# Kernel optimization log

Measured on AMD Instinct MI355X. Metric: run time of the kernel, lower is better.

The kernel has to match this reference:

```python
import jax, jax.numpy as jnp
import numpy as np

D, R, C = 4, 6, 32
P = 2 * R + 1          # 13 (both pixel patch and memory patch, since memory_patch_R == R)
N = P * P              # 169
DIL_INT = 15


def corr_sampler(f1, f2, p, dil):
    """SpatialCorrelationSampler(kernel_size=1, patch_size=p, dilation_patch=dil).
    out[b,i,j,y,x] = sum_c f1[b,c,y,x] * f2[b,c, y+(i-Rp)*dil, x+(j-Rp)*dil] (zero pad)."""
    Rp = (p - 1) // 2
    pad = Rp * dil
    b, c, h, w = f1.shape
    f2p = jnp.pad(f2, ((0, 0), (0, 0), (pad, pad), (pad, pad)))
    outs = [jnp.einsum('bchw,bchw->bhw', f1, f2p[:, :, i * dil:i * dil + h, j * dil:j * dil + w])
            for i in range(p) for j in range(p)]
    return jnp.stack(outs, 1).reshape(b, p, p, h, w)


def bilinear_gather(im, ys, xs):
    """Bilinear sample im [b,c,H,W] at float coords ys,xs [b,N,h,w]; zeros outside."""
    H, W = im.shape[2], im.shape[3]
    y0 = jnp.floor(ys)
    x0 = jnp.floor(xs)
    wy = ys - y0
    wx = xs - x0

    def g(yi, xi):
        valid = ((yi >= 0) & (yi < H) & (xi >= 0) & (xi < W)).astype(im.dtype)
        yc = jnp.clip(yi, 0, H - 1).astype(jnp.int32)
        xc = jnp.clip(xi, 0, W - 1).astype(jnp.int32)
        out = jax.vmap(lambda imb, yb, xb: imb[:, yb, xb])(im, yc, xc)  # [b,c,N,h,w]
        return out * valid[:, None]

    return (g(y0, x0) * ((1 - wy) * (1 - wx))[:, None]
            + g(y0, x0 + 1) * ((1 - wy) * wx)[:, None]
            + g(y0 + 1, x0) * (wy * (1 - wx))[:, None]
            + g(y0 + 1, x0 + 1) * (wy * wx)[:, None])


def deform_im2col(im, offset, p):
    """Deformable im2col: for each output pixel (y,x) and kernel pos (ky,kx),
    bilinearly sample im at (y+ky-Rp+off_y, x+kx-Rp+off_x). offset [...,0]=x, [...,1]=y.
    Returns [b,c,p*p,h,w]."""
    b, c, h, w = im.shape
    Rp = (p - 1) // 2
    ky, kx = jnp.meshgrid(jnp.arange(p) - Rp, jnp.arange(p) - Rp, indexing='ij')
    ky = ky.reshape(-1).astype(im.dtype)
    kx = kx.reshape(-1).astype(im.dtype)
    ys = (jnp.arange(h, dtype=im.dtype)[None, None, :, None]
          + ky[None, :, None, None] + offset[..., 1][:, None])  # [b,N,h,w]
    xs = (jnp.arange(w, dtype=im.dtype)[None, None, None, :]
          + kx[None, :, None, None] + offset[..., 0][:, None])
    return bilinear_gather(im, ys, xs)


def unfold_patches(x, p, pad):
    """F.unfold(kernel_size=p, padding=pad) -> [b,c,p*p,h,w]."""
    b, c, h, w = x.shape
    xp = jnp.pad(x, ((0, 0), (0, 0), (pad, pad), (pad, pad)))
    cols = [xp[:, :, i:i + h, j:j + w] for i in range(p) for j in range(p)]
    return jnp.stack(cols, 2)


def _forward(feats_r, feats_t, quantized_r, ref_index, current_ind):
    ri = np.asarray(ref_index)
    ci = int(current_ind)
    diffs = [ci - int(x) for x in ri]
    nsearch = sum(1 for d in diffs if d > DIL_INT)
    dirates = [min(4, d // DIL_INT + 1) for d in diffs if d > DIL_INT]
    nref = feats_r.shape[0]
    b, c, h, w = feats_t.shape

    # offset grid: _y,_x = meshgrid(ij) so grid[...,0]=x-offset, grid[...,1]=y-offset
    _y, _x = jnp.meshgrid(jnp.arange(-R, R + 1), jnp.arange(-R, R + 1), indexing='ij')
    grid = jnp.stack([_x, _y], -1).astype(feats_t.dtype)  # [P,P,2]

    corrs_pixel = []
    offset0 = []
    for s in range(nsearch):
        cc = corr_sampler(feats_t, feats_r[s], P, dirates[s])             # [b,P,P,h,w]
        soft = jax.nn.softmax(cc.reshape(b, N, h * w), axis=1).reshape(b, P, P, h, w)
        off = jnp.einsum('bijhw,ijd->bhwd', soft, grid) * dirates[s]      # [b,h,w,2]
        offset0.append(off)
        col0 = deform_im2col(feats_r[s], off, P)                          # [b,c,N,h,w]
        corrs_pixel.append(jnp.einsum('bchw,bcnhw->bnhw', feats_t, col0).reshape(b, N, h * w))
    for ind in range(nsearch, nref):
        corrs_pixel.append(corr_sampler(feats_t, feats_r[ind], P, 1).reshape(b, N, h * w))

    corr_pixel = jax.nn.softmax(jnp.concatenate(corrs_pixel, 1), axis=1)  # [b,nref*N,h*w]

    # prep: float + stride-D subsampling (C-channel input, so no one-hot branch)
    qr = [quantized_r[i][:, :, ::D, ::D] for i in range(nref)]            # [b,C,h,w]
    cols = [deform_im2col(qr[i], offset0[i], P).reshape(b, C, N, h * w) for i in range(nsearch)]
    cols += [unfold_patches(qr[i], P, R).reshape(b, C, N, h * w) for i in range(nsearch, nref)]
    image_uf = jnp.concatenate(cols, 2)                                   # [b,C,nref*N,h*w]

    out = jnp.einsum('bkl,bckl->bcl', corr_pixel, image_uf).reshape(b, C, h, w)
    return out


def setup_inputs() -> dict:
    key = jax.random.key(0)
    k1, k2, k3 = jax.random.split(key, 3)
    feats_r = jax.random.normal(k1, (3, 1, 64, 56, 56), jnp.float32) * 0.2
    feats_t = jax.random.normal(k2, (1, 64, 56, 56), jnp.float32) * 0.2
    quantized_r = jax.random.uniform(k3, (3, 1, 32, 224, 224), jnp.float32)
    return {
        'feats_r': feats_r,
        'feats_t': feats_t,
        'quantized_r': quantized_r,
        'ref_index': np.array([0, 30, 39], dtype=np.int64),
        'current_ind': 40,
    }


def reference(feats_r, feats_t, quantized_r, ref_index, current_ind):
    return _forward(feats_r, feats_t, quantized_r, ref_index, current_ind)
```

## Files before the change

### kernel.cpp

```cpp
#include <hip/hip_runtime.h>

#define HW   56
#define NPIX 3136
#define CH   64
#define CQ   32
#define PS   13
#define NPOS 169
#define GS   14
#define NG   196

typedef __attribute__((ext_vector_type(8))) short short8;
typedef __attribute__((ext_vector_type(4))) float f32x4;

__device__ inline float warpMax(float v) {
#pragma unroll
  for (int o = 32; o > 0; o >>= 1) v = fmaxf(v, __shfl_xor(v, o));
  return v;
}
__device__ inline float warpSum(float v) {
#pragma unroll
  for (int o = 32; o > 0; o >>= 1) v += __shfl_xor(v, o);
  return v;
}
__device__ inline ushort f2bf(float f) {
  unsigned u = __float_as_uint(f);
  return (ushort)((u + 0x7fffu + ((u >> 16) & 1u)) >> 16);
}

__global__ __launch_bounds__(256) void prep_all(
    const float* __restrict__ ft_in,
    const float* __restrict__ fr_in,
    const float* __restrict__ q_in,
    ushort* __restrict__ ft_out,
    ushort* __restrict__ fr_out,
    float* __restrict__ qout,
    float* __restrict__ zrow) {
  __shared__ float smem[CQ * (HW + 1)];
  int bid = blockIdx.x, tid = threadIdx.x;
  if (bid < 784) {
    if (bid == 0 && tid < 64) zrow[tid] = 0.f;
    int m = bid / 196, t = bid - m * 196;
    int row0 = (t / 98) * 32;
    int col0 = (t - (t / 98) * 98) * 32;
    const float* src = (m == 0) ? ft_in : fr_in + (size_t)(m - 1) * CH * NPIX;
    ushort* dst      = (m == 0) ? ft_out : fr_out + (size_t)(m - 1) * NPIX * CH;
    int tx = tid & 31, ty = tid >> 5;
    for (int r = ty; r < 32; r += 8)
      smem[r * 33 + tx] = src[(size_t)(row0 + r) * NPIX + col0 + tx];
    __syncthreads();
    for (int r = ty; r < 32; r += 8)
      dst[(size_t)(col0 + r) * CH + row0 + tx] = f2bf(smem[tx * 33 + r]);
  } else {
    int q = bid - 784;
    int r = q / HW, yy = q - r * HW;
    for (int idx = tid; idx < CQ * HW; idx += 256) {
      int c = idx / HW, xx = idx - c * HW;
      smem[c * (HW + 1) + xx] = q_in[((size_t)(r * CQ + c) * 224 + yy * 4) * 224 + xx * 4];
    }
    __syncthreads();
    for (int idx = tid; idx < CQ * HW; idx += 256) {
      int xx = idx >> 5, c = idx & 31;
      qout[(size_t)r * NPIX * CQ + (size_t)(yy * HW + xx) * CQ + c] = smem[c * (HW + 1) + xx];
    }
  }
}

__global__ __launch_bounds__(256, 6) void colorizer_main(
    const ushort* __restrict__ ftb,
    const ushort* __restrict__ frb,
    const float*  __restrict__ qr,
    const ushort* __restrict__ zrow,
    float* __restrict__ out)
{
  __shared__ float s_cc[176];
  __shared__ float s_e[528];
  __shared__ float s_D[208];
  __shared__ float s_wg[224];
  __shared__ int   s_offg[224];
  __shared__ int   s_off2[192];
  __shared__ f32x4 s_pf[32];
  __shared__ float r_max1[4], r_sum1[12], r_max2[4], r_sum2[4];

  int pix = blockIdx.x;
  int y = pix / HW, x = pix - y * HW;
  int tid = threadIdx.x;
  int wid = tid >> 6, lane = tid & 63;
  int mrow = lane & 15;
  int klane = lane >> 4;

  if (tid < 16) { s_offg[208 + tid] = -1; s_off2[176 + tid] = -1; }

  const ushort* frb0 = frb;
  const ushort* frb1 = frb + (size_t)NPIX * CH;
  const ushort* frb2 = frb + (size_t)2 * NPIX * CH;
  const f32x4* qr0v = (const f32x4*)qr;
  const f32x4* qr1v = qr0v + (size_t)NPIX * 8;
  const f32x4* qr2v = qr0v + (size_t)2 * NPIX * 8;

  const ushort* fb = ftb + (size_t)pix * CH;
  const ushort* plo = (mrow == 0) ? (fb + klane * 8) : zrow;
  const ushort* phi = (mrow == 0) ? (fb + 32 + klane * 8) : zrow;
  short8 b_lo = *(const short8*)plo;
  short8 b_hi = *(const short8*)phi;

  for (int g = wid; g < 11; g += 4) {
    int d = g * 16 + mrow;
    int ii = d / PS, jj = d - ii * PS;
    int sy1 = y + (ii - 6) * 3, sx1 = x + (jj - 6) * 3;
    int sy2 = y + ii - 6,        sx2 = x + jj - 6;
    bool dv = d < NPOS;
    bool v1 = dv && ((unsigned)sy1 < HW) && ((unsigned)sx1 < HW);
    bool v2 = dv && ((unsigned)sy2 < HW) && ((unsigned)sx2 < HW);
    int ro2 = sy2 * HW + sx2;
    const ushort* rb0 = v1 ? (frb0 + (size_t)(sy1 * HW + sx1) * CH) : zrow;
    const ushort* rb1 = v2 ? (frb1 + (size_t)ro2 * CH) : zrow;
    const ushort* rb2 = v2 ? (frb2 + (size_t)ro2 * CH) : zrow;
    short8 a0lo = *(const short8*)(rb0 + klane * 8);
    short8 a0hi = *(const short8*)(rb0 + 32 + klane * 8);
    short8 a1lo = *(const short8*)(rb1 + klane * 8);
    short8 a1hi = *(const short8*)(rb1 + 32 + klane * 8);
    short8 a2lo = *(const short8*)(rb2 + klane * 8);
    short8 a2hi = *(const short8*)(rb2 + 32 + klane * 8);
    f32x4 acc0 = {0.f, 0.f, 0.f, 0.f}, acc1 = acc0, acc2 = acc0;
    acc0 = __builtin_amdgcn_mfma_f32_16x16x32_bf16(a0lo, b_lo, acc0, 0, 0, 0);
    acc0 = __builtin_amdgcn_mfma_f32_16x16x32_bf16(a0hi, b_hi, acc0, 0, 0, 0);
    acc1 = __builtin_amdgcn_mfma_f32_16x16x32_bf16(a1lo, b_lo, acc1, 0, 0, 0);
    acc1 = __builtin_amdgcn_mfma_f32_16x16x32_bf16(a1hi, b_hi, acc1, 0, 0, 0);
    acc2 = __builtin_amdgcn_mfma_f32_16x16x32_bf16(a2lo, b_lo, acc2, 0, 0, 0);
    acc2 = __builtin_amdgcn_mfma_f32_16x16x32_bf16(a2hi, b_hi, acc2, 0, 0, 0);
    if (klane == 0) s_off2[d] = v2 ? ro2 : -1;
    if (mrow == 0) {
      *(f32x4*)&s_cc[g * 16 + klane * 4]        = acc0;
      *(f32x4*)&s_e[176 + g * 16 + klane * 4]   = acc1;
      *(f32x4*)&s_e[352 + g * 16 + klane * 4]   = acc2;
    }
  }
  __syncthreads();

  int pi = tid / PS, pj = tid - (tid / PS) * PS;
  float cc = (tid < NPOS) ? s_cc[tid] : -1e30f;
  float wmx = warpMax(cc);
  if (lane == 0) r_max1[wid] = wmx;
  __syncthreads();
  float m1 = fmaxf(fmaxf(r_max1[0], r_max1[1]), fmaxf(r_max1[2], r_max1[3]));
  float e1 = (tid < NPOS) ? __expf(cc - m1) : 0.f;
  float a0 = warpSum(e1);
  float a1 = warpSum((tid < NPOS) ? e1 * (float)(pj - 6) : 0.f);
  float a2 = warpSum((tid < NPOS) ? e1 * (float)(pi - 6) : 0.f);
  if (lane == 0) { r_sum1[wid] = a0; r_sum1[4 + wid] = a1; r_sum1[8 + wid] = a2; }
  __syncthreads();
  float se  = r_sum1[0] + r_sum1[1] + r_sum1[2] + r_sum1[3];
  float sxe = r_sum1[4] + r_sum1[5] + r_sum1[6] + r_sum1[7];
  float sye = r_sum1[8] + r_sum1[9] + r_sum1[10] + r_sum1[11];
  float offx = 3.f * sxe / se;
  float offy = 3.f * sye / se;

  float fy0 = floorf(offy), fx0 = floorf(offx);
  int   iy0 = (int)fy0,     ix0 = (int)fx0;
  float wy = offy - fy0,    wx = offx - fx0;
  float w00 = (1.f - wy) * (1.f - wx), w01 = (1.f - wy) * wx;
  float w10 = wy * (1.f - wx),         w11 = wy * wx;

  for (int g = wid; g < 13; g += 8) {
    int gB = g + 4;
    bool hasB = gB < 13;
    int d = g * 16 + mrow;
    int a = d / GS, bq = d - a * GS;
    int sy = y + iy0 + a - 6, sx = x + ix0 + bq - 6;
    bool vA = (d < NG) && ((unsigned)sy < HW) && ((unsigned)sx < HW);
    int roA = sy * HW + sx;
    const ushort* rbA = vA ? (frb0 + (size_t)roA * CH) : zrow;
    int dB = gB * 16 + mrow;
    int aB = dB / GS, bB = dB - aB * GS;
    int syB = y + iy0 + aB - 6, sxB = x + ix0 + bB - 6;
    bool vB = hasB && (dB < NG) && ((unsigned)syB < HW) && ((unsigned)sxB < HW);
    int roB = syB * HW + sxB;
    const ushort* rbB = vB ? (frb0 + (size_t)roB * CH) : zrow;
    short8 aAlo = *(const short8*)(rbA + klane * 8);
    short8 aAhi = *(const short8*)(rbA + 32 + klane * 8);
    short8 aBlo = *(const short8*)(rbB + klane * 8);
    short8 aBhi = *(const short8*)(rbB + 32 + klane * 8);
    f32x4 accA = {0.f, 0.f, 0.f, 0.f}, accB = accA;
    accA = __builtin_amdgcn_mfma_f32_16x16x32_bf16(aAlo, b_lo, accA, 0, 0, 0);
    accA = __builtin_amdgcn_mfma_f32_16x16x32_bf16(aAhi, b_hi, accA, 0, 0, 0);
    accB = __builtin_amdgcn_mfma_f32_16x16x32_bf16(aBlo, b_lo, accB, 0, 0, 0);
    accB = __builtin_amdgcn_mfma_f32_16x16x32_bf16(aBhi, b_hi, accB, 0, 0, 0);
    if (klane == 0) s_offg[d] = vA ? roA : -1;
    if (mrow == 0) *(f32x4*)&s_D[g * 16 + klane * 4] = accA;
    if (hasB) {
      if (klane == 0) s_offg[dB] = vB ? roB : -1;
      if (mrow == 0) *(f32x4*)&s_D[gB * 16 + klane * 4] = accB;
    }
  }
  __syncthreads();

  if (tid < NPOS)
    s_e[tid] = w00 * s_D[pi * GS + pj]       + w01 * s_D[pi * GS + pj + 1]
             + w10 * s_D[(pi + 1) * GS + pj] + w11 * s_D[(pi + 1) * GS + pj + 1];
  if (tid < 7) { s_e[169 + tid] = -1e30f; s_e[345 + tid] = -1e30f; s_e[521 + tid] = -1e30f; }
  __syncthreads();

  float v = fmaxf(s_e[tid], s_e[tid + 256]);
  if (tid < 16) v = fmaxf(v, s_e[512 + tid]);
  float wm = warpMax(v);
  if (lane == 0) r_max2[wid] = wm;
  __syncthreads();
  float m2 = fmaxf(fmaxf(r_max2[0], r_max2[1]), fmaxf(r_max2[2], r_max2[3]));
  float e_a = __expf(s_e[tid] - m2);
  float e_b = __expf(s_e[tid + 256] - m2);
  float e_c = (tid < 16) ? __expf(s_e[512 + tid] - m2) : 0.f;
  s_e[tid] = e_a; s_e[tid + 256] = e_b;
  if (tid < 16) s_e[512 + tid] = e_c;
  float wsum = warpSum(e_a + e_b + e_c);
  if (lane == 0) r_sum2[wid] = wsum;
  __syncthreads();
  float S = r_sum2[0] + r_sum2[1] + r_sum2[2] + r_sum2[3];

  if (tid < NG) {
    int a = tid / GS, b = tid - (tid / GS) * GS;
    float acc = 0.f;
    if (a < PS && b < PS) acc += w00 * s_e[a * PS + b];
    if (a < PS && b >= 1) acc += w01 * s_e[a * PS + b - 1];
    if (a >= 1 && b < PS) acc += w10 * s_e[(a - 1) * PS + b];
    if (a >= 1 && b >= 1) acc += w11 * s_e[(a - 1) * PS + b - 1];
    s_wg[tid] = acc;
  }
  __syncthreads();

  int slot = tid >> 3, ln = tid & 7;
  f32x4 acc = {0.f, 0.f, 0.f, 0.f};
#pragma unroll
  for (int k = 0; k < 7; ++k) {
    int d = slot + k * 32;
    int ro = s_offg[d];
    if (ro >= 0) {
      float w = s_wg[d];
      f32x4 qv = qr0v[(size_t)ro * 8 + ln];
      acc.x = fmaf(w, qv.x, acc.x); acc.y = fmaf(w, qv.y, acc.y);
      acc.z = fmaf(w, qv.z, acc.z); acc.w = fmaf(w, qv.w, acc.w);
    }
  }
#pragma unroll
  for (int k = 0; k < 6; ++k) {
    int d = slot + k * 32;
    int ro = s_off2[d];
    if (ro >= 0) {
      float w1 = s_e[176 + d], w2 = s_e[352 + d];
      f32x4 q1 = qr1v[(size_t)ro * 8 + ln];
      f32x4 q2 = qr2v[(size_t)ro * 8 + ln];
      acc.x = fmaf(w1, q1.x, acc.x); acc.y = fmaf(w1, q1.y, acc.y);
      acc.z = fmaf(w1, q1.z, acc.z); acc.w = fmaf(w1, q1.w, acc.w);
      acc.x = fmaf(w2, q2.x, acc.x); acc.y = fmaf(w2, q2.y, acc.y);
      acc.z = fmaf(w2, q2.z, acc.z); acc.w = fmaf(w2, q2.w, acc.w);
    }
  }
#pragma unroll
  for (int o = 8; o <= 32; o <<= 1) {
    acc.x += __shfl_xor(acc.x, o);
    acc.y += __shfl_xor(acc.y, o);
    acc.z += __shfl_xor(acc.z, o);
    acc.w += __shfl_xor(acc.w, o);
  }
  if (lane < 8) s_pf[wid * 8 + lane] = acc;
  __syncthreads();
  if (tid < 8) {
    f32x4 t = s_pf[tid];
    f32x4 u = s_pf[8 + tid];
    t.x += u.x; t.y += u.y; t.z += u.z; t.w += u.w;
    u = s_pf[16 + tid];
    t.x += u.x; t.y += u.y; t.z += u.z; t.w += u.w;
    u = s_pf[24 + tid];
    t.x += u.x; t.y += u.y; t.z += u.z; t.w += u.w;
    float inv = 1.f / S;
    out[(size_t)(4 * tid + 0) * NPIX + pix] = t.x * inv;
    out[(size_t)(4 * tid + 1) * NPIX + pix] = t.y * inv;
    out[(size_t)(4 * tid + 2) * NPIX + pix] = t.z * inv;
    out[(size_t)(4 * tid + 3) * NPIX + pix] = t.w * inv;
  }
}

extern "C" void kernel_launch(void* const* d_in, const int* in_sizes, int n_in,
                              void* d_out, int out_size, void* d_ws, size_t ws_size,
                              hipStream_t stream) {
  const float* feats_r     = (const float*)d_in[0];
  const float* feats_t     = (const float*)d_in[1];
  const float* quantized_r = (const float*)d_in[2];

  ushort* ftb = (ushort*)d_ws;
  ushort* frb = ftb + 200704;
  float*  qr  = (float*)(frb + 602112);
  float*  zro = qr + 301056;

  prep_all<<<952, 256, 0, stream>>>(feats_t, feats_r, quantized_r,
                                    ftb, frb, qr, zro);
  colorizer_main<<<NPIX, 256, 0, stream>>>(ftb, frb, qr, (const ushort*)zro,
                                           (float*)d_out);
}
```

Before: 51.69 us.

## Map one pixel per wavefront instead of per block, removing block barriers

Each wavefront now processes a whole output pixel, with four pixels per 256-thread block and a private shared-memory region per wave. All block-level __syncthreads and cross-wave reductions are replaced by wave-local shuffles and an lgkmcnt wait, so one pixel no longer stalls four waves at repeated barriers. The trade-off is more serial work per wave: fully unrolled MFMA and gather loops over 11, 13, 28 and 24 iterations, which raises register pressure. The launch bound was lowered from 6 to 4 to allow for this. Occupancy drops, and latency hiding now depends on overlap between waves rather than work split within a block.

Measured after the change: 55.61 us. 1.08x slower.

```diff
diff --git a/kernel.cpp b/kernel.cpp
--- a/kernel.cpp
+++ b/kernel.cpp
@@ -12,19 +12,14 @@
 typedef __attribute__((ext_vector_type(8))) short short8;
 typedef __attribute__((ext_vector_type(4))) float f32x4;
 
-__device__ inline float warpMax(float v) {
-#pragma unroll
-  for (int o = 32; o > 0; o >>= 1) v = fmaxf(v, __shfl_xor(v, o));
-  return v;
-}
-__device__ inline float warpSum(float v) {
-#pragma unroll
-  for (int o = 32; o > 0; o >>= 1) v += __shfl_xor(v, o);
-  return v;
-}
 __device__ inline ushort f2bf(float f) {
   unsigned u = __float_as_uint(f);
   return (ushort)((u + 0x7fffu + ((u >> 16) & 1u)) >> 16);
+}
+
+__device__ inline void wave_sync() {
+  asm volatile("s_waitcnt lgkmcnt(0)" ::: "memory");
+  __builtin_amdgcn_sched_barrier(0);
 }
 
 __global__ __launch_bounds__(256) void prep_all(
@@ -65,30 +60,38 @@
   }
 }
 
-__global__ __launch_bounds__(256, 6) void colorizer_main(
+#define WB_E    0
+#define WB_D    528
+#define WB_WG   736
+#define WB_OFFG 960
+#define WB_OFF2 1184
+#define WB_SIZE 1376
+
+__global__ __launch_bounds__(256, 4) void colorizer_main(
     const ushort* __restrict__ ftb,
     const ushort* __restrict__ frb,
     const float*  __restrict__ qr,
     const ushort* __restrict__ zrow,
     float* __restrict__ out)
 {
-  __shared__ float s_cc[176];
-  __shared__ float s_e[528];
-  __shared__ float s_D[208];
-  __shared__ float s_wg[224];
-  __shared__ int   s_offg[224];
-  __shared__ int   s_off2[192];
-  __shared__ f32x4 s_pf[32];
-  __shared__ float r_max1[4], r_sum1[12], r_max2[4], r_sum2[4];
-
-  int pix = blockIdx.x;
-  int y = pix / HW, x = pix - y * HW;
+  __shared__ int smem[4 * WB_SIZE];
+
   int tid = threadIdx.x;
   int wid = tid >> 6, lane = tid & 63;
+  int pix = blockIdx.x * 4 + wid;
+  int y = pix / HW, x = pix - y * HW;
   int mrow = lane & 15;
   int klane = lane >> 4;
 
-  if (tid < 16) { s_offg[208 + tid] = -1; s_off2[176 + tid] = -1; }
+  int*   wb   = smem + wid * WB_SIZE;
+  float* e    = (float*)(wb + WB_E);
+  float* D    = (float*)(wb + WB_D);
+  float* wg   = (float*)(wb + WB_WG);
+  int*   offg = wb + WB_OFFG;
+  float* cc   = (float*)offg;
+  int*   off2 = wb + WB_OFF2;
+
+  if (lane < 16) { offg[208 + lane] = -1; off2[176 + lane] = -1; }
 
   const ushort* frb0 = frb;
   const ushort* frb1 = frb + (size_t)NPIX * CH;
@@ -103,7 +106,8 @@
   short8 b_lo = *(const short8*)plo;
   short8 b_hi = *(const short8*)phi;
 
-  for (int g = wid; g < 11; g += 4) {
+#pragma unroll
+  for (int g = 0; g < 11; ++g) {
     int d = g * 16 + mrow;
     int ii = d / PS, jj = d - ii * PS;
     int sy1 = y + (ii - 6) * 3, sx1 = x + (jj - 6) * 3;
@@ -128,124 +132,146 @@
     acc1 = __builtin_amdgcn_mfma_f32_16x16x32_bf16(a1hi, b_hi, acc1, 0, 0, 0);
     acc2 = __builtin_amdgcn_mfma_f32_16x16x32_bf16(a2lo, b_lo, acc2, 0, 0, 0);
     acc2 = __builtin_amdgcn_mfma_f32_16x16x32_bf16(a2hi, b_hi, acc2, 0, 0, 0);
-    if (klane == 0) s_off2[d] = v2 ? ro2 : -1;
+    if (klane == 0) off2[d] = v2 ? ro2 : -1;
     if (mrow == 0) {
-      *(f32x4*)&s_cc[g * 16 + klane * 4]        = acc0;
-      *(f32x4*)&s_e[176 + g * 16 + klane * 4]   = acc1;
-      *(f32x4*)&s_e[352 + g * 16 + klane * 4]   = acc2;
-    }
-  }
-  __syncthreads();
-
-  int pi = tid / PS, pj = tid - (tid / PS) * PS;
-  float cc = (tid < NPOS) ? s_cc[tid] : -1e30f;
-  float wmx = warpMax(cc);
-  if (lane == 0) r_max1[wid] = wmx;
-  __syncthreads();
-  float m1 = fmaxf(fmaxf(r_max1[0], r_max1[1]), fmaxf(r_max1[2], r_max1[3]));
-  float e1 = (tid < NPOS) ? __expf(cc - m1) : 0.f;
-  float a0 = warpSum(e1);
-  float a1 = warpSum((tid < NPOS) ? e1 * (float)(pj - 6) : 0.f);
-  float a2 = warpSum((tid < NPOS) ? e1 * (float)(pi - 6) : 0.f);
-  if (lane == 0) { r_sum1[wid] = a0; r_sum1[4 + wid] = a1; r_sum1[8 + wid] = a2; }
-  __syncthreads();
-  float se  = r_sum1[0] + r_sum1[1] + r_sum1[2] + r_sum1[3];
-  float sxe = r_sum1[4] + r_sum1[5] + r_sum1[6] + r_sum1[7];
-  float sye = r_sum1[8] + r_sum1[9] + r_sum1[10] + r_sum1[11];
+      *(f32x4*)&cc[g * 16 + klane * 4]      = acc0;
+      *(f32x4*)&e[176 + g * 16 + klane * 4] = acc1;
+      *(f32x4*)&e[352 + g * 16 + klane * 4] = acc2;
+    }
+  }
+  wave_sync();
+
+  float vs[3];
+  float mx = -1e30f;
+#pragma unroll
+  for (int k = 0; k < 3; ++k) {
+    int id = lane + 64 * k;
+    float c = (id < NPOS) ? cc[id] : -1e30f;
+    vs[k] = c;
+    mx = fmaxf(mx, c);
+  }
+#pragma unroll
+  for (int o = 1; o < 64; o <<= 1) mx = fmaxf(mx, __shfl_xor(mx, o));
+  float se = 0.f, sxe = 0.f, sye = 0.f;
+#pragma unroll
+  for (int k = 0; k < 3; ++k) {
+    int id = lane + 64 * k;
+    if (id < NPOS) {
+      float ex = __expf(vs[k] - mx);
+      int pi = id / PS, pj = id - pi * PS;
+      se += ex;
+      sxe += ex * (float)(pj - 6);
+      sye += ex * (float)(pi - 6);
+    }
+  }
+#pragma unroll
+  for (int o = 1; o < 64; o <<= 1) {
+    se  += __shfl_xor(se, o);
+    sxe += __shfl_xor(sxe, o);
+    sye += __shfl_xor(sye, o);
+  }
   float offx = 3.f * sxe / se;
   float offy = 3.f * sye / se;
 
   float fy0 = floorf(offy), fx0 = floorf(offx);
   int   iy0 = (int)fy0,     ix0 = (int)fx0;
-  float wy = offy - fy0,    wx = offx - fx0;
-  float w00 = (1.f - wy) * (1.f - wx), w01 = (1.f - wy) * wx;
-  float w10 = wy * (1.f - wx),         w11 = wy * wx;
-
-  for (int g = wid; g < 13; g += 8) {
-    int gB = g + 4;
-    bool hasB = gB < 13;
+  float wyf = offy - fy0,   wxf = offx - fx0;
+  float w00 = (1.f - wyf) * (1.f - wxf), w01 = (1.f - wyf) * wxf;
+  float w10 = wyf * (1.f - wxf),         w11 = wyf * wxf;
+
+#pragma unroll
+  for (int g = 0; g < 13; ++g) {
     int d = g * 16 + mrow;
     int a = d / GS, bq = d - a * GS;
     int sy = y + iy0 + a - 6, sx = x + ix0 + bq - 6;
     bool vA = (d < NG) && ((unsigned)sy < HW) && ((unsigned)sx < HW);
     int roA = sy * HW + sx;
     const ushort* rbA = vA ? (frb0 + (size_t)roA * CH) : zrow;
-    int dB = gB * 16 + mrow;
-    int aB = dB / GS, bB = dB - aB * GS;
-    int syB = y + iy0 + aB - 6, sxB = x + ix0 + bB - 6;
-    bool vB = hasB && (dB < NG) && ((unsigned)syB < HW) && ((unsigned)sxB < HW);
-    int roB = syB * HW + sxB;
-    const ushort* rbB = vB ? (frb0 + (size_t)roB * CH) : zrow;
     short8 aAlo = *(const short8*)(rbA + klane * 8);
     short8 aAhi = *(const short8*)(rbA + 32 + klane * 8);
-    short8 aBlo = *(const short8*)(rbB + klane * 8);
-    short8 aBhi = *(const short8*)(rbB + 32 + klane * 8);
-    f32x4 accA = {0.f, 0.f, 0.f, 0.f}, accB = accA;
+    f32x4 accA = {0.f, 0.f, 0.f, 0.f};
     accA = __builtin_amdgcn_mfma_f32_16x16x32_bf16(aAlo, b_lo, accA, 0, 0, 0);
     accA = __builtin_amdgcn_mfma_f32_16x16x32_bf16(aAhi, b_hi, accA, 0, 0, 0);
-    accB = __builtin_amdgcn_mfma_f32_16x16x32_bf16(aBlo, b_lo, accB, 0, 0, 0);
-    accB = __builtin_amdgcn_mfma_f32_16x16x32_bf16(aBhi, b_hi, accB, 0, 0, 0);
-    if (klane == 0) s_offg[d] = vA ? roA : -1;
-    if (mrow == 0) *(f32x4*)&s_D[g * 16 + klane * 4] = accA;
-    if (hasB) {
-      if (klane == 0) s_offg[dB] = vB ? roB : -1;
-      if (mrow == 0) *(f32x4*)&s_D[gB * 16 + klane * 4] = accB;
-    }
-  }
-  __syncthreads();
-
-  if (tid < NPOS)
-    s_e[tid] = w00 * s_D[pi * GS + pj]       + w01 * s_D[pi * GS + pj + 1]
-             + w10 * s_D[(pi + 1) * GS + pj] + w11 * s_D[(pi + 1) * GS + pj + 1];
-  if (tid < 7) { s_e[169 + tid] = -1e30f; s_e[345 + tid] = -1e30f; s_e[521 + tid] = -1e30f; }
-  __syncthreads();
-
-  float v = fmaxf(s_e[tid], s_e[tid + 256]);
-  if (tid < 16) v = fmaxf(v, s_e[512 + tid]);
-  float wm = warpMax(v);
-  if (lane == 0) r_max2[wid] = wm;
-  __syncthreads();
-  float m2 = fmaxf(fmaxf(r_max2[0], r_max2[1]), fmaxf(r_max2[2], r_max2[3]));
-  float e_a = __expf(s_e[tid] - m2);
-  float e_b = __expf(s_e[tid + 256] - m2);
-  float e_c = (tid < 16) ? __expf(s_e[512 + tid] - m2) : 0.f;
-  s_e[tid] = e_a; s_e[tid + 256] = e_b;
-  if (tid < 16) s_e[512 + tid] = e_c;
-  float wsum = warpSum(e_a + e_b + e_c);
-  if (lane == 0) r_sum2[wid] = wsum;
-  __syncthreads();
-  float S = r_sum2[0] + r_sum2[1] + r_sum2[2] + r_sum2[3];
-
-  if (tid < NG) {
-    int a = tid / GS, b = tid - (tid / GS) * GS;
-    float acc = 0.f;
-    if (a < PS && b < PS) acc += w00 * s_e[a * PS + b];
-    if (a < PS && b >= 1) acc += w01 * s_e[a * PS + b - 1];
-    if (a >= 1 && b < PS) acc += w10 * s_e[(a - 1) * PS + b];
-    if (a >= 1 && b >= 1) acc += w11 * s_e[(a - 1) * PS + b - 1];
-    s_wg[tid] = acc;
-  }
-  __syncthreads();
-
-  int slot = tid >> 3, ln = tid & 7;
+    if (klane == 0) offg[d] = vA ? roA : -1;
+    if (mrow == 0) *(f32x4*)&D[g * 16 + klane * 4] = accA;
+  }
+  wave_sync();
+
+#pragma unroll
+  for (int k = 0; k < 3; ++k) {
+    int id = lane + 64 * k;
+    if (id < NPOS) {
+      int pi = id / PS, pj = id - (id / PS) * PS;
+      e[id] = w00 * D[pi * GS + pj]       + w01 * D[pi * GS + pj + 1]
+            + w10 * D[(pi + 1) * GS + pj] + w11 * D[(pi + 1) * GS + pj + 1];
+    } else if (id < 176) {
+      e[id] = -1e30f;
+    }
+  }
+  if (lane < 7) { e[345 + lane] = -1e30f; e[521 + lane] = -1e30f; }
+  wave_sync();
+
+  float vv[8];
+  float mx2 = -1e30f;
+#pragma unroll
+  for (int k = 0; k < 8; ++k) { vv[k] = e[lane + 64 * k]; mx2 = fmaxf(mx2, vv[k]); }
+  float vex = (lane < 16) ? e[512 + lane] : -1e30f;
+  mx2 = fmaxf(mx2, vex);
+#pragma unroll
+  for (int o = 1; o < 64; o <<= 1) mx2 = fmaxf(mx2, __shfl_xor(mx2, o));
+  float ps = 0.f;
+#pragma unroll
+  for (int k = 0; k < 8; ++k) {
+    float ex = __expf(vv[k] - mx2);
+    e[lane + 64 * k] = ex;
+    ps += ex;
+  }
+  if (lane < 16) {
+    float ex = __expf(vex - mx2);
+    e[512 + lane] = ex;
+    ps += ex;
+  }
+#pragma unroll
+  for (int o = 1; o < 64; o <<= 1) ps += __shfl_xor(ps, o);
+  float S = ps;
+  wave_sync();
+
+#pragma unroll
+  for (int k = 0; k < 4; ++k) {
+    int t = lane + 64 * k;
+    if (t < 224) {
+      float acc = 0.f;
+      if (t < NG) {
+        int a = t / GS, b = t - (t / GS) * GS;
+        if (a < PS && b < PS) acc += w00 * e[a * PS + b];
+        if (a < PS && b >= 1) acc += w01 * e[a * PS + b - 1];
+        if (a >= 1 && b < PS) acc += w10 * e[(a - 1) * PS + b];
+        if (a >= 1 && b >= 1) acc += w11 * e[(a - 1) * PS + b - 1];
+      }
+      wg[t] = acc;
+    }
+  }
+  wave_sync();
+
+  int slot = lane >> 3, ln = lane & 7;
   f32x4 acc = {0.f, 0.f, 0.f, 0.f};
 #pragma unroll
-  for (int k = 0; k < 7; ++k) {
-    int d = slot + k * 32;
-    int ro = s_offg[d];
+  for (int k = 0; k < 28; ++k) {
+    int d = slot + k * 8;
+    int ro = offg[d];
     if (ro >= 0) {
-      float w = s_wg[d];
+      float w = wg[d];
       f32x4 qv = qr0v[(size_t)ro * 8 + ln];
       acc.x = fmaf(w, qv.x, acc.x); acc.y = fmaf(w, qv.y, acc.y);
       acc.z = fmaf(w, qv.z, acc.z); acc.w = fmaf(w, qv.w, acc.w);
     }
   }
 #pragma unroll
-  for (int k = 0; k < 6; ++k) {
-    int d = slot + k * 32;
-    int ro = s_off2[d];
+  for (int k = 0; k < 24; ++k) {
+    int d = slot + k * 8;
+    int ro = off2[d];
     if (ro >= 0) {
-      float w1 = s_e[176 + d], w2 = s_e[352 + d];
+      float w1 = e[176 + d], w2 = e[352 + d];
       f32x4 q1 = qr1v[(size_t)ro * 8 + ln];
       f32x4 q2 = qr2v[(size_t)ro * 8 + ln];
       acc.x = fmaf(w1, q1.x, acc.x); acc.y = fmaf(w1, q1.y, acc.y);
@@ -261,21 +287,12 @@
     acc.z += __shfl_xor(acc.z, o);
     acc.w += __shfl_xor(acc.w, o);
   }
-  if (lane < 8) s_pf[wid * 8 + lane] = acc;
-  __syncthreads();
-  if (tid < 8) {
-    f32x4 t = s_pf[tid];
-    f32x4 u = s_pf[8 + tid];
-    t.x += u.x; t.y += u.y; t.z += u.z; t.w += u.w;
-    u = s_pf[16 + tid];
-    t.x += u.x; t.y += u.y; t.z += u.z; t.w += u.w;
-    u = s_pf[24 + tid];
-    t.x += u.x; t.y += u.y; t.z += u.z; t.w += u.w;
+  if (lane < 8) {
     float inv = 1.f / S;
-    out[(size_t)(4 * tid + 0) * NPIX + pix] = t.x * inv;
-    out[(size_t)(4 * tid + 1) * NPIX + pix] = t.y * inv;
-    out[(size_t)(4 * tid + 2) * NPIX + pix] = t.z * inv;
-    out[(size_t)(4 * tid + 3) * NPIX + pix] = t.w * inv;
+    out[(size_t)(4 * ln + 0) * NPIX + pix] = acc.x * inv;
+    out[(size_t)(4 * ln + 1) * NPIX + pix] = acc.y * inv;
+    out[(size_t)(4 * ln + 2) * NPIX + pix] = acc.z * inv;
+    out[(size_t)(4 * ln + 3) * NPIX + pix] = acc.w * inv;
   }
 }
 
@@ -293,6 +310,6 @@
 
   prep_all<<<952, 256, 0, stream>>>(feats_t, feats_r, quantized_r,
                                     ftb, frb, qr, zro);
-  colorizer_main<<<NPIX, 256, 0, stream>>>(ftb, frb, qr, (const ushort*)zro,
-                                           (float*)d_out);
-}
+  colorizer_main<<<NPIX / 4, 256, 0, stream>>>(ftb, frb, qr, (const ushort*)zro,
+                                               (float*)d_out);
+}
```
